# Kernel tuning notes

Measured on AMD Instinct MI355X. Metric: run time of the kernel, lower is better.

The kernel has to match this reference:

```python
import jax, jax.numpy as jnp
import numpy as np

LN_EPS = 1e-5


def _ssm_scan(x_ssm, A, Bm, C, reverse):
    # x_ssm: [B, L, d_inner]; A, Bm, C: [d_inner, d_state]
    Bb, L, di = x_ssm.shape
    ds = Bm.shape[1]

    def step(h, x_t):
        # h: [B, d_inner, d_state], x_t: [B, d_inner]
        h = jnp.clip(h * A[None] + x_t[:, :, None] * Bm[None], -10.0, 10.0)
        y = jnp.einsum('bid,id->bi', h, C)
        return h, y

    h0 = jnp.zeros((Bb, di, ds), x_ssm.dtype)
    _, ys = jax.lax.scan(step, h0, jnp.swapaxes(x_ssm, 0, 1), reverse=reverse)
    return jnp.swapaxes(ys, 0, 1)  # [B, L, d_inner], time-ordered


def setup_inputs() -> dict:
    key = jax.random.key(0)
    ks = jax.random.split(key, 6)
    B, L, D = 4, 2048, 1024
    d_state, expand = 16, 2
    d_inner = D * expand
    x = jax.random.normal(ks[0], (B, L, D), jnp.float32)
    # xavier-ish scaled params
    in_proj_w = jax.random.normal(ks[1], (d_inner * 2, D), jnp.float32) * np.float32(1.0 / np.sqrt(D))
    A_log = jax.random.normal(ks[2], (d_inner, d_state), jnp.float32)
    B_mat = jax.random.normal(ks[3], (d_inner, d_state), jnp.float32) * np.float32(1.0 / np.sqrt(d_state))
    C_mat = jnp.full((d_inner, d_state), 0.01, jnp.float32)
    out_proj_w = jax.random.normal(ks[4], (D, d_inner), jnp.float32) * np.float32(1.0 / np.sqrt(d_inner))
    ln_w = jnp.ones((D,), jnp.float32)
    ln_b = jnp.zeros((D,), jnp.float32)
    return {"x": x, "in_proj_w": in_proj_w, "A_log": A_log, "B_mat": B_mat,
            "C_mat": C_mat, "out_proj_w": out_proj_w, "ln_w": ln_w, "ln_b": ln_b}


def reference(x, in_proj_w, A_log, B_mat, C_mat, out_proj_w, ln_w, ln_b):
    # LayerNorm
    mu = jnp.mean(x, axis=-1, keepdims=True)
    var = jnp.mean((x - mu) ** 2, axis=-1, keepdims=True)
    xn = (x - mu) * jax.lax.rsqrt(var + LN_EPS) * ln_w + ln_b
    # in_proj (no bias), split into ssm stream and gate
    x_proj = jnp.einsum('bld,ed->ble', xn, in_proj_w)  # [B, L, 2*d_inner]
    x_ssm, gate = jnp.split(x_proj, 2, axis=-1)
    # A = -clamp(exp(A_log), -10, -0.01)  (saturates to 0.01, kept faithfully)
    A = -jnp.clip(jnp.exp(A_log), -10.0, -0.01)
    out_f = _ssm_scan(x_ssm, A, B_mat, C_mat, reverse=False)
    out_b = _ssm_scan(x_ssm, A, B_mat, C_mat, reverse=True)
    out = (out_f + out_b) * 0.5 * jax.nn.silu(gate)
    return jnp.einsum('bli,di->bld', out, out_proj_w)
```

## Files before the change

kernel.cpp:

```cpp
#include <hip/hip_runtime.h>

typedef __attribute__((ext_vector_type(8))) _Float16 f16x8;
typedef __attribute__((ext_vector_type(4))) float f32x4;

#define GLOBAL_AS __attribute__((address_space(1)))
#define LDS_AS __attribute__((address_space(3)))

static constexpr int Bb = 4, LL = 2048, DD = 1024, DI = 2048, DS = 16;
static constexpr int MROWS = Bb * LL;
static constexpr int N1 = 2 * DI;
static constexpr int K1 = DD;
static constexpr int N2 = DD;
static constexpr int K2 = DI;

__device__ __forceinline__ unsigned short f2h(float f) {
  _Float16 h = (_Float16)f;
  union { _Float16 h; unsigned short u; } c; c.h = h;
  return c.u;
}
__device__ __forceinline__ float h2f(unsigned short u) {
  union { unsigned short u; _Float16 h; } c; c.u = u;
  return (float)c.h;
}

__global__ __launch_bounds__(256) void ln_half_kernel(
    const float* __restrict__ x, const float* __restrict__ lnw,
    const float* __restrict__ lnb, unsigned short* __restrict__ A1) {
  const int r = blockIdx.x;
  const int tid = threadIdx.x;
  const float4 v = reinterpret_cast<const float4*>(x + (size_t)r * DD)[tid];
  float s = v.x + v.y + v.z + v.w;
#pragma unroll
  for (int off = 32; off >= 1; off >>= 1) s += __shfl_xor(s, off, 64);
  __shared__ float red[8];
  const int wid = tid >> 6;
  if ((tid & 63) == 0) red[wid] = s;
  __syncthreads();
  const float mu = (red[0] + red[1] + red[2] + red[3]) * (1.0f / DD);
  const float dx = v.x - mu, dy = v.y - mu, dz = v.z - mu, dw = v.w - mu;
  float ss = dx * dx + dy * dy + dz * dz + dw * dw;
#pragma unroll
  for (int off = 32; off >= 1; off >>= 1) ss += __shfl_xor(ss, off, 64);
  if ((tid & 63) == 0) red[4 + wid] = ss;
  __syncthreads();
  const float var = (red[4] + red[5] + red[6] + red[7]) * (1.0f / DD);
  const float rs = rsqrtf(var + 1e-5f);
  const float4 w4 = reinterpret_cast<const float4*>(lnw)[tid];
  const float4 b4 = reinterpret_cast<const float4*>(lnb)[tid];
  ushort4 h4;
  h4.x = f2h(dx * rs * w4.x + b4.x);
  h4.y = f2h(dy * rs * w4.y + b4.y);
  h4.z = f2h(dz * rs * w4.z + b4.z);
  h4.w = f2h(dw * rs * w4.w + b4.w);
  *reinterpret_cast<ushort4*>(&A1[(size_t)r * DD + tid * 4]) = h4;
}

__global__ __launch_bounds__(256) void f32_to_f16_kernel(
    const float* __restrict__ W, unsigned short* __restrict__ O) {
  const int gid = blockIdx.x * 256 + threadIdx.x;
  const float4 w = reinterpret_cast<const float4*>(W)[gid];
  ushort4 h4;
  h4.x = f2h(w.x); h4.y = f2h(w.y); h4.z = f2h(w.z); h4.w = f2h(w.w);
  reinterpret_cast<ushort4*>(O)[gid] = h4;
}

__global__ __launch_bounds__(512, 2) void gemm_bt_256(
    const unsigned short* __restrict__ A, const unsigned short* __restrict__ B,
    unsigned short* __restrict__ C, int M, int N, int K) {
  __shared__ unsigned short sm[2][2][256 * 64];
  const int tid = threadIdx.x;
  const int wid = tid >> 6;
  const int lane = tid & 63;
  const int wm = wid >> 2;
  const int wn = wid & 3;
  const int mt = M >> 8;
  const int cpx = gridDim.x >> 3;
  const int bid = blockIdx.x;
  const int sw = (bid & 7) * cpx + (bid >> 3);
  const int bm = sw % mt;
  const int bn = sw / mt;
  const size_t arow0 = (size_t)bm * 256;
  const size_t brow0 = (size_t)bn * 256;

  const unsigned short* gA[4];
  const unsigned short* gB[4];
#pragma unroll
  for (int j = 0; j < 4; ++j) {
    const int idx = j * 512 + tid;
    const int prow = idx >> 3;
    const int scol = ((idx & 7) ^ (prow & 7)) << 3;
    gA[j] = A + (arow0 + prow) * (size_t)K + scol;
    gB[j] = B + (brow0 + prow) * (size_t)K + scol;
  }
  auto stageA = [&](int buf) {
#pragma unroll
    for (int j = 0; j < 4; ++j) {
      __builtin_amdgcn_global_load_lds((const GLOBAL_AS void*)gA[j],
          (LDS_AS void*)&sm[buf][0][(j * 512 + (wid << 6)) * 8], 16, 0, 0);
      gA[j] += 64;
    }
  };
  auto stageB = [&](int buf) {
#pragma unroll
    for (int j = 0; j < 4; ++j) {
      __builtin_amdgcn_global_load_lds((const GLOBAL_AS void*)gB[j],
          (LDS_AS void*)&sm[buf][1][(j * 512 + (wid << 6)) * 8], 16, 0, 0);
      gB[j] += 64;
    }
  };

  const int q = lane >> 4;
  const int l7 = lane & 7;
  const int fr = lane & 15;
  int swz[2];
  swz[0] = (q << 3) ^ (l7 << 3);
  swz[1] = (32 + (q << 3)) ^ (l7 << 3);

  int arows[8], brows[4];
#pragma unroll
  for (int mf = 0; mf < 8; ++mf) arows[mf] = ((wm << 7) + mf * 16 + fr) * 64;
#pragma unroll
  for (int nf = 0; nf < 4; ++nf) brows[nf] = ((wn << 6) + nf * 16 + fr) * 64;

  f32x4 acc[8][4] = {};

  const int NTK = K >> 6;
  stageA(0);
  stageB(0);
  __syncthreads();

  for (int t = 0; t < NTK; ++t) {
    const int cur = t & 1, nxt = cur ^ 1;
    if (t + 1 < NTK) { stageA(nxt); stageB(nxt); }
    f16x8 af[8][2], bf[4][2];
#pragma unroll
    for (int mf = 0; mf < 8; ++mf)
#pragma unroll
      for (int ks = 0; ks < 2; ++ks)
        af[mf][ks] = *reinterpret_cast<const f16x8*>(&sm[cur][0][arows[mf] + swz[ks]]);
#pragma unroll
    for (int nf = 0; nf < 4; ++nf)
#pragma unroll
      for (int ks = 0; ks < 2; ++ks)
        bf[nf][ks] = *reinterpret_cast<const f16x8*>(&sm[cur][1][brows[nf] + swz[ks]]);
#pragma unroll
    for (int ks = 0; ks < 2; ++ks)
#pragma unroll
      for (int mf = 0; mf < 8; ++mf)
#pragma unroll
        for (int nf = 0; nf < 4; ++nf)
          acc[mf][nf] = __builtin_amdgcn_mfma_f32_16x16x32_f16(
              af[mf][ks], bf[nf][ks], acc[mf][nf], 0, 0, 0);
    __syncthreads();
  }

  const int fcol = lane & 15;
  const int frow4 = (lane >> 4) << 2;
#pragma unroll
  for (int mf = 0; mf < 8; ++mf)
#pragma unroll
    for (int nf = 0; nf < 4; ++nf) {
      const size_t row0 = arow0 + (wm << 7) + mf * 16 + frow4;
      const size_t col = brow0 + (wn << 6) + nf * 16 + fcol;
#pragma unroll
      for (int j = 0; j < 4; ++j)
        C[(row0 + j) * (size_t)N + col] = f2h(acc[mf][nf][j]);
    }
}

__global__ __launch_bounds__(512, 2) void gemm_bt_256n128(
    const unsigned short* __restrict__ A, const unsigned short* __restrict__ B,
    float* __restrict__ C, int M, int N, int K) {
  __shared__ unsigned short sm[2][24576];
  const int tid = threadIdx.x;
  const int wid = tid >> 6;
  const int lane = tid & 63;
  const int wm = wid >> 2;
  const int wn = wid & 3;
  const int mt = M >> 8;
  const int cpx = gridDim.x >> 3;
  const int bid = blockIdx.x;
  const int sw = (bid & 7) * cpx + (bid >> 3);
  const int bm = sw % mt;
  const int bn = sw / mt;
  const size_t arow0 = (size_t)bm * 256;
  const size_t brow0 = (size_t)bn * 128;

  const unsigned short* gA[4];
  const unsigned short* gB[2];
#pragma unroll
  for (int j = 0; j < 4; ++j) {
    const int idx = j * 512 + tid;
    const int prow = idx >> 3;
    const int scol = ((idx & 7) ^ (prow & 7)) << 3;
    gA[j] = A + (arow0 + prow) * (size_t)K + scol;
  }
#pragma unroll
  for (int j = 0; j < 2; ++j) {
    const int idx = j * 512 + tid;
    const int prow = idx >> 3;
    const int scol = ((idx & 7) ^ (prow & 7)) << 3;
    gB[j] = B + (brow0 + prow) * (size_t)K + scol;
  }
  auto stageA = [&](int buf) {
#pragma unroll
    for (int j = 0; j < 4; ++j) {
      __builtin_amdgcn_global_load_lds((const GLOBAL_AS void*)gA[j],
          (LDS_AS void*)&sm[buf][(j * 512 + (wid << 6)) * 8], 16, 0, 0);
      gA[j] += 64;
    }
  };
  auto stageB = [&](int buf) {
#pragma unroll
    for (int j = 0; j < 2; ++j) {
      __builtin_amdgcn_global_load_lds((const GLOBAL_AS void*)gB[j],
          (LDS_AS void*)&sm[buf][16384 + (j * 512 + (wid << 6)) * 8], 16, 0, 0);
      gB[j] += 64;
    }
  };

  const int q = lane >> 4;
  const int l7 = lane & 7;
  const int fr = lane & 15;
  int swz[2];
  swz[0] = (q << 3) ^ (l7 << 3);
  swz[1] = (32 + (q << 3)) ^ (l7 << 3);

  int arows[8], brows[2];
#pragma unroll
  for (int mf = 0; mf < 8; ++mf) arows[mf] = ((wm << 7) + mf * 16 + fr) * 64;
#pragma unroll
  for (int nf = 0; nf < 2; ++nf) brows[nf] = 16384 + ((wn << 5) + nf * 16 + fr) * 64;

  f32x4 acc[8][2] = {};

  const int NTK = K >> 6;
  stageA(0);
  stageB(0);
  __syncthreads();

  for (int t = 0; t < NTK; ++t) {
    const int cur = t & 1, nxt = cur ^ 1;
    if (t + 1 < NTK) { stageA(nxt); stageB(nxt); }
    f16x8 af[8][2], bf[2][2];
#pragma unroll
    for (int mf = 0; mf < 8; ++mf)
#pragma unroll
      for (int ks = 0; ks < 2; ++ks)
        af[mf][ks] = *reinterpret_cast<const f16x8*>(&sm[cur][arows[mf] + swz[ks]]);
#pragma unroll
    for (int nf = 0; nf < 2; ++nf)
#pragma unroll
      for (int ks = 0; ks < 2; ++ks)
        bf[nf][ks] = *reinterpret_cast<const f16x8*>(&sm[cur][brows[nf] + swz[ks]]);
#pragma unroll
    for (int ks = 0; ks < 2; ++ks)
#pragma unroll
      for (int mf = 0; mf < 8; ++mf)
#pragma unroll
        for (int nf = 0; nf < 2; ++nf)
          acc[mf][nf] = __builtin_amdgcn_mfma_f32_16x16x32_f16(
              af[mf][ks], bf[nf][ks], acc[mf][nf], 0, 0, 0);
    __syncthreads();
  }

  const int fcol = lane & 15;
  const int frow4 = (lane >> 4) << 2;
#pragma unroll
  for (int mf = 0; mf < 8; ++mf)
#pragma unroll
    for (int nf = 0; nf < 2; ++nf) {
      const size_t row0 = arow0 + (wm << 7) + mf * 16 + frow4;
      const size_t col = brow0 + (wn << 5) + nf * 16 + fcol;
#pragma unroll
      for (int j = 0; j < 4; ++j)
        C[(row0 + j) * (size_t)N + col] = acc[mf][nf][j];
    }
}

__global__ __launch_bounds__(256) void scan_kernel(
    const unsigned short* __restrict__ xp, const float* __restrict__ Bm,
    const float* __restrict__ Cm, unsigned short* __restrict__ oss) {
  constexpr int T = 32, KH = 8;
  const int blk = blockIdx.x;
  const int igrp = blk & 3;
  const int c = (blk >> 2) & 63;
  const int b = blk >> 8;
  const int tid = threadIdx.x;
  const int i0 = igrp * 512 + tid * 2;
  float d0 = 0.f, d1 = 0.f;
#pragma unroll
  for (int ch = 0; ch < 2; ++ch) {
    const float4* bp = reinterpret_cast<const float4*>(Bm + (size_t)(i0 + ch) * DS);
    const float4* cp = reinterpret_cast<const float4*>(Cm + (size_t)(i0 + ch) * DS);
    float d = 0.f;
#pragma unroll
    for (int qv = 0; qv < 4; ++qv) {
      const float4 bv = bp[qv], cv = cp[qv];
      d += bv.x * cv.x + bv.y * cv.y + bv.z * cv.z + bv.w * cv.w;
    }
    if (ch == 0) d0 = d; else d1 = d;
  }
  const float dh0 = 0.5f * d0, dh1 = 0.5f * d1;
  const int t0 = c * T;
  const size_t rowbase = (size_t)b * LL;
  float yf0[T], yf1[T];
  float g0 = 0.f, g1 = 0.f;
  {
    const int hstart = (t0 >= KH) ? t0 - KH : 0;
    for (int t = hstart; t < t0; ++t) {
      const unsigned int u = *reinterpret_cast<const unsigned int*>(
          xp + (rowbase + t) * (size_t)N1 + i0);
      g0 = fmaf(0.01f, g0, h2f((unsigned short)(u & 0xffff)));
      g1 = fmaf(0.01f, g1, h2f((unsigned short)(u >> 16)));
    }
#pragma unroll
    for (int j = 0; j < T; ++j) {
      const unsigned int u = *reinterpret_cast<const unsigned int*>(
          xp + (rowbase + t0 + j) * (size_t)N1 + i0);
      g0 = fmaf(0.01f, g0, h2f((unsigned short)(u & 0xffff)));
      g1 = fmaf(0.01f, g1, h2f((unsigned short)(u >> 16)));
      yf0[j] = g0; yf1[j] = g1;
    }
  }
  g0 = 0.f; g1 = 0.f;
  {
    const int tend = (t0 + T - 1 + KH <= LL - 1) ? (t0 + T - 1 + KH) : (LL - 1);
    for (int t = tend; t >= t0 + T; --t) {
      const unsigned int u = *reinterpret_cast<const unsigned int*>(
          xp + (rowbase + t) * (size_t)N1 + i0);
      g0 = fmaf(0.01f, g0, h2f((unsigned short)(u & 0xffff)));
      g1 = fmaf(0.01f, g1, h2f((unsigned short)(u >> 16)));
    }
#pragma unroll
    for (int j = T - 1; j >= 0; --j) {
      const size_t row = rowbase + t0 + j;
      const unsigned int u = *reinterpret_cast<const unsigned int*>(
          xp + row * (size_t)N1 + i0);
      g0 = fmaf(0.01f, g0, h2f((unsigned short)(u & 0xffff)));
      g1 = fmaf(0.01f, g1, h2f((unsigned short)(u >> 16)));
      const unsigned int ug = *reinterpret_cast<const unsigned int*>(
          xp + row * (size_t)N1 + DI + i0);
      const float gt0 = h2f((unsigned short)(ug & 0xffff));
      const float gt1 = h2f((unsigned short)(ug >> 16));
      const float sg0 = gt0 / (1.f + expf(-gt0));
      const float sg1 = gt1 / (1.f + expf(-gt1));
      const float o0 = (yf0[j] + g0) * dh0 * sg0;
      const float o1 = (yf1[j] + g1) * dh1 * sg1;
      const unsigned int up = (unsigned int)f2h(o0) | ((unsigned int)f2h(o1) << 16);
      *reinterpret_cast<unsigned int*>(oss + row * (size_t)DI + i0) = up;
    }
  }
}

extern "C" void kernel_launch(void* const* d_in, const int* in_sizes, int n_in,
                              void* d_out, int out_size, void* d_ws, size_t ws_size,
                              hipStream_t stream) {
  (void)in_sizes; (void)n_in; (void)out_size; (void)ws_size;
  const float* x          = (const float*)d_in[0];
  const float* in_proj_w  = (const float*)d_in[1];
  const float* B_mat      = (const float*)d_in[3];
  const float* C_mat      = (const float*)d_in[4];
  const float* out_proj_w = (const float*)d_in[5];
  const float* ln_w       = (const float*)d_in[6];
  const float* ln_b       = (const float*)d_in[7];
  float* out = (float*)d_out;

  char* ws = (char*)d_ws;
  unsigned short* A1  = (unsigned short*)ws; ws += (size_t)MROWS * K1 * 2;
  unsigned short* B1  = (unsigned short*)ws; ws += (size_t)N1 * K1 * 2;
  unsigned short* B2  = (unsigned short*)ws; ws += (size_t)N2 * K2 * 2;
  unsigned short* OSS = (unsigned short*)ws; ws += (size_t)MROWS * DI * 2;
  unsigned short* XP  = (unsigned short*)ws; ws += (size_t)MROWS * N1 * 2;

  f32_to_f16_kernel<<<dim3((N1 * K1 / 4) / 256), dim3(256), 0, stream>>>(in_proj_w, B1);
  f32_to_f16_kernel<<<dim3((N2 * K2 / 4) / 256), dim3(256), 0, stream>>>(out_proj_w, B2);
  ln_half_kernel<<<dim3(MROWS), dim3(256), 0, stream>>>(x, ln_w, ln_b, A1);
  gemm_bt_256<<<dim3((MROWS / 256) * (N1 / 256)), dim3(512), 0, stream>>>(A1, B1, XP, MROWS, N1, K1);
  scan_kernel<<<dim3(1024), dim3(256), 0, stream>>>(XP, B_mat, C_mat, OSS);
  gemm_bt_256n128<<<dim3((MROWS / 256) * (N2 / 128)), dim3(512), 0, stream>>>(OSS, B2, out, MROWS, N2, K2);
}
```

Measured before the change: 188.3 us.

## Move linear SSM filter before in_proj and fuse gating into GEMM epilogue

Because the scan is linear and time-invariant, the bidirectional filter is applied to the normalized input (width 1024) before the in-projection instead of to the projected stream (width 2048). The B·C scale is folded into the converted in_proj weights. The new fused GEMM loads both the filtered and unfiltered inputs with a paired weight tile and computes the SiLU gate and product in its epilogue through LDS. This removes the half-precision XP round trip and the separate scan kernel's read of it. In exchange it adds a smaller filter pass and a GEMM that stages three operands per K step.

```diff
diff --git a/kernel.cpp b/kernel.cpp
--- a/kernel.cpp
+++ b/kernel.cpp
@@ -55,6 +55,26 @@
   *reinterpret_cast<ushort4*>(&A1[(size_t)r * DD + tid * 4]) = h4;
 }
 
+__global__ __launch_bounds__(256) void wconv1_kernel(
+    const float* __restrict__ W, const float* __restrict__ Bm,
+    const float* __restrict__ Cm, unsigned short* __restrict__ B1) {
+  const int n = blockIdx.x;
+  const int tid = threadIdx.x;
+  float scale = 1.f;
+  if (n < DI) {
+    float d = 0.f;
+#pragma unroll
+    for (int s = 0; s < DS; ++s)
+      d += Bm[(size_t)n * DS + s] * Cm[(size_t)n * DS + s];
+    scale = 0.5f * d;
+  }
+  const float4 w = reinterpret_cast<const float4*>(W + (size_t)n * DD)[tid];
+  ushort4 h4;
+  h4.x = f2h(w.x * scale); h4.y = f2h(w.y * scale);
+  h4.z = f2h(w.z * scale); h4.w = f2h(w.w * scale);
+  reinterpret_cast<ushort4*>(B1 + (size_t)n * DD)[tid] = h4;
+}
+
 __global__ __launch_bounds__(256) void f32_to_f16_kernel(
     const float* __restrict__ W, unsigned short* __restrict__ O) {
   const int gid = blockIdx.x * 256 + threadIdx.x;
@@ -64,108 +84,179 @@
   reinterpret_cast<ushort4*>(O)[gid] = h4;
 }
 
-__global__ __launch_bounds__(512, 2) void gemm_bt_256(
-    const unsigned short* __restrict__ A, const unsigned short* __restrict__ B,
-    unsigned short* __restrict__ C, int M, int N, int K) {
-  __shared__ unsigned short sm[2][2][256 * 64];
+__global__ __launch_bounds__(256) void filter_kernel(
+    const unsigned short* __restrict__ xn, unsigned short* __restrict__ xs) {
+  constexpr int T = 32, KH = 8;
+  const int blk = blockIdx.x;
+  const int igrp = blk & 1;
+  const int c = (blk >> 1) & 63;
+  const int b = blk >> 7;
+  const int tid = threadIdx.x;
+  const int i0 = igrp * 512 + tid * 2;
+  const int t0 = c * T;
+  const size_t rowbase = (size_t)b * LL;
+  float yf0[T], yf1[T];
+  float g0 = 0.f, g1 = 0.f;
+  {
+    const int hstart = (t0 >= KH) ? t0 - KH : 0;
+    for (int t = hstart; t < t0; ++t) {
+      const unsigned int u = *reinterpret_cast<const unsigned int*>(
+          xn + (rowbase + t) * (size_t)DD + i0);
+      g0 = fmaf(0.01f, g0, h2f((unsigned short)(u & 0xffff)));
+      g1 = fmaf(0.01f, g1, h2f((unsigned short)(u >> 16)));
+    }
+#pragma unroll
+    for (int j = 0; j < T; ++j) {
+      const unsigned int u = *reinterpret_cast<const unsigned int*>(
+          xn + (rowbase + t0 + j) * (size_t)DD + i0);
+      g0 = fmaf(0.01f, g0, h2f((unsigned short)(u & 0xffff)));
+      g1 = fmaf(0.01f, g1, h2f((unsigned short)(u >> 16)));
+      yf0[j] = g0; yf1[j] = g1;
+    }
+  }
+  g0 = 0.f; g1 = 0.f;
+  {
+    const int tend = (t0 + T - 1 + KH <= LL - 1) ? (t0 + T - 1 + KH) : (LL - 1);
+    for (int t = tend; t >= t0 + T; --t) {
+      const unsigned int u = *reinterpret_cast<const unsigned int*>(
+          xn + (rowbase + t) * (size_t)DD + i0);
+      g0 = fmaf(0.01f, g0, h2f((unsigned short)(u & 0xffff)));
+      g1 = fmaf(0.01f, g1, h2f((unsigned short)(u >> 16)));
+    }
+#pragma unroll
+    for (int j = T - 1; j >= 0; --j) {
+      const size_t row = rowbase + t0 + j;
+      const unsigned int u = *reinterpret_cast<const unsigned int*>(
+          xn + row * (size_t)DD + i0);
+      g0 = fmaf(0.01f, g0, h2f((unsigned short)(u & 0xffff)));
+      g1 = fmaf(0.01f, g1, h2f((unsigned short)(u >> 16)));
+      const unsigned int up =
+          (unsigned int)f2h(yf0[j] + g0) | ((unsigned int)f2h(yf1[j] + g1) << 16);
+      *reinterpret_cast<unsigned int*>(xs + row * (size_t)DD + i0) = up;
+    }
+  }
+}
+
+__global__ __launch_bounds__(512, 2) void gemm_fused(
+    const unsigned short* __restrict__ XS, const unsigned short* __restrict__ XN,
+    const unsigned short* __restrict__ W, unsigned short* __restrict__ OSS) {
+  __shared__ unsigned short sm[2][3][8192];
   const int tid = threadIdx.x;
   const int wid = tid >> 6;
   const int lane = tid & 63;
   const int wm = wid >> 2;
   const int wn = wid & 3;
-  const int mt = M >> 8;
+  const int mt = MROWS >> 8;
   const int cpx = gridDim.x >> 3;
   const int bid = blockIdx.x;
   const int sw = (bid & 7) * cpx + (bid >> 3);
   const int bm = sw % mt;
   const int bn = sw / mt;
   const size_t arow0 = (size_t)bm * 256;
-  const size_t brow0 = (size_t)bn * 256;
-
-  const unsigned short* gA[4];
-  const unsigned short* gB[4];
-#pragma unroll
-  for (int j = 0; j < 4; ++j) {
+
+  const unsigned short* gXS[2];
+  const unsigned short* gXN[2];
+  const unsigned short* gW[2];
+#pragma unroll
+  for (int j = 0; j < 2; ++j) {
     const int idx = j * 512 + tid;
-    const int prow = idx >> 3;
-    const int scol = ((idx & 7) ^ (prow & 7)) << 3;
-    gA[j] = A + (arow0 + prow) * (size_t)K + scol;
-    gB[j] = B + (brow0 + prow) * (size_t)K + scol;
-  }
-  auto stageA = [&](int buf) {
-#pragma unroll
-    for (int j = 0; j < 4; ++j) {
-      __builtin_amdgcn_global_load_lds((const GLOBAL_AS void*)gA[j],
-          (LDS_AS void*)&sm[buf][0][(j * 512 + (wid << 6)) * 8], 16, 0, 0);
-      gA[j] += 64;
+    const int prow = idx >> 2;
+    const int scol = ((idx & 3) ^ ((prow >> 1) & 3)) << 3;
+    gXS[j] = XS + (arow0 + prow) * (size_t)K1 + scol;
+    gXN[j] = XN + (arow0 + prow) * (size_t)K1 + scol;
+    const int brow = (prow < 128) ? (bn * 128 + prow)
+                                  : (DI + bn * 128 + (prow - 128));
+    gW[j] = W + (size_t)brow * K1 + scol;
+  }
+  auto stage = [&](int buf) {
+#pragma unroll
+    for (int j = 0; j < 2; ++j) {
+      __builtin_amdgcn_global_load_lds((const GLOBAL_AS void*)gXS[j],
+          (LDS_AS void*)&sm[buf][0][(j * 512 + tid) * 8], 16, 0, 0);
+      gXS[j] += 32;
+    }
+#pragma unroll
+    for (int j = 0; j < 2; ++j) {
+      __builtin_amdgcn_global_load_lds((const GLOBAL_AS void*)gXN[j],
+          (LDS_AS void*)&sm[buf][1][(j * 512 + tid) * 8], 16, 0, 0);
+      gXN[j] += 32;
+    }
+#pragma unroll
+    for (int j = 0; j < 2; ++j) {
+      __builtin_amdgcn_global_load_lds((const GLOBAL_AS void*)gW[j],
+          (LDS_AS void*)&sm[buf][2][(j * 512 + tid) * 8], 16, 0, 0);
+      gW[j] += 32;
     }
   };
-  auto stageB = [&](int buf) {
-#pragma unroll
-    for (int j = 0; j < 4; ++j) {
-      __builtin_amdgcn_global_load_lds((const GLOBAL_AS void*)gB[j],
-          (LDS_AS void*)&sm[buf][1][(j * 512 + (wid << 6)) * 8], 16, 0, 0);
-      gB[j] += 64;
-    }
-  };
 
   const int q = lane >> 4;
-  const int l7 = lane & 7;
   const int fr = lane & 15;
-  int swz[2];
-  swz[0] = (q << 3) ^ (l7 << 3);
-  swz[1] = (32 + (q << 3)) ^ (l7 << 3);
+  const int swzk = ((q ^ ((fr >> 1) & 3)) << 3);
+  const int areg = (wn >= 2) ? 1 : 0;
 
   int arows[8], brows[4];
 #pragma unroll
-  for (int mf = 0; mf < 8; ++mf) arows[mf] = ((wm << 7) + mf * 16 + fr) * 64;
-#pragma unroll
-  for (int nf = 0; nf < 4; ++nf) brows[nf] = ((wn << 6) + nf * 16 + fr) * 64;
+  for (int mf = 0; mf < 8; ++mf) arows[mf] = ((wm << 7) + mf * 16 + fr) * 32;
+#pragma unroll
+  for (int nf = 0; nf < 4; ++nf) brows[nf] = ((wn << 6) + nf * 16 + fr) * 32;
 
   f32x4 acc[8][4] = {};
 
-  const int NTK = K >> 6;
-  stageA(0);
-  stageB(0);
+  const int NTK = K1 >> 5;
+  stage(0);
   __syncthreads();
 
   for (int t = 0; t < NTK; ++t) {
     const int cur = t & 1, nxt = cur ^ 1;
-    if (t + 1 < NTK) { stageA(nxt); stageB(nxt); }
-    f16x8 af[8][2], bf[4][2];
-#pragma unroll
-    for (int mf = 0; mf < 8; ++mf)
-#pragma unroll
-      for (int ks = 0; ks < 2; ++ks)
-        af[mf][ks] = *reinterpret_cast<const f16x8*>(&sm[cur][0][arows[mf] + swz[ks]]);
+    if (t + 1 < NTK) stage(nxt);
+    f16x8 af[8], bf[4];
+#pragma unroll
+    for (int mf = 0; mf < 8; ++mf)
+      af[mf] = *reinterpret_cast<const f16x8*>(&sm[cur][areg][arows[mf] + swzk]);
 #pragma unroll
     for (int nf = 0; nf < 4; ++nf)
-#pragma unroll
-      for (int ks = 0; ks < 2; ++ks)
-        bf[nf][ks] = *reinterpret_cast<const f16x8*>(&sm[cur][1][brows[nf] + swz[ks]]);
-#pragma unroll
-    for (int ks = 0; ks < 2; ++ks)
-#pragma unroll
-      for (int mf = 0; mf < 8; ++mf)
-#pragma unroll
-        for (int nf = 0; nf < 4; ++nf)
-          acc[mf][nf] = __builtin_amdgcn_mfma_f32_16x16x32_f16(
-              af[mf][ks], bf[nf][ks], acc[mf][nf], 0, 0, 0);
+      bf[nf] = *reinterpret_cast<const f16x8*>(&sm[cur][2][brows[nf] + swzk]);
+#pragma unroll
+    for (int mf = 0; mf < 8; ++mf)
+#pragma unroll
+      for (int nf = 0; nf < 4; ++nf)
+        acc[mf][nf] = __builtin_amdgcn_mfma_f32_16x16x32_f16(
+            af[mf], bf[nf], acc[mf][nf], 0, 0, 0);
     __syncthreads();
   }
 
+  unsigned short* gl = &sm[0][0][0];
   const int fcol = lane & 15;
   const int frow4 = (lane >> 4) << 2;
-#pragma unroll
-  for (int mf = 0; mf < 8; ++mf)
-#pragma unroll
-    for (int nf = 0; nf < 4; ++nf) {
-      const size_t row0 = arow0 + (wm << 7) + mf * 16 + frow4;
-      const size_t col = brow0 + (wn << 6) + nf * 16 + fcol;
-#pragma unroll
-      for (int j = 0; j < 4; ++j)
-        C[(row0 + j) * (size_t)N + col] = f2h(acc[mf][nf][j]);
-    }
+  if (wn >= 2) {
+#pragma unroll
+    for (int mf = 0; mf < 8; ++mf)
+#pragma unroll
+      for (int nf = 0; nf < 4; ++nf) {
+        const int gcol = ((wn - 2) << 6) + nf * 16 + fcol;
+        const int r0 = (wm << 7) + mf * 16 + frow4;
+#pragma unroll
+        for (int j = 0; j < 4; ++j) {
+          const float g = acc[mf][nf][j];
+          gl[(r0 + j) * 132 + gcol] = f2h(g / (1.f + expf(-g)));
+        }
+      }
+  }
+  __syncthreads();
+  if (wn < 2) {
+#pragma unroll
+    for (int mf = 0; mf < 8; ++mf)
+#pragma unroll
+      for (int nf = 0; nf < 4; ++nf) {
+        const int scol = (wn << 6) + nf * 16 + fcol;
+        const int r0 = (wm << 7) + mf * 16 + frow4;
+#pragma unroll
+        for (int j = 0; j < 4; ++j) {
+          const float o = acc[mf][nf][j] * h2f(gl[(r0 + j) * 132 + scol]);
+          OSS[(arow0 + r0 + j) * (size_t)DI + bn * 128 + scol] = f2h(o);
+        }
+      }
+  }
 }
 
 __global__ __launch_bounds__(512, 2) void gemm_bt_256n128(
@@ -278,81 +369,6 @@
     }
 }
 
-__global__ __launch_bounds__(256) void scan_kernel(
-    const unsigned short* __restrict__ xp, const float* __restrict__ Bm,
-    const float* __restrict__ Cm, unsigned short* __restrict__ oss) {
-  constexpr int T = 32, KH = 8;
-  const int blk = blockIdx.x;
-  const int igrp = blk & 3;
-  const int c = (blk >> 2) & 63;
-  const int b = blk >> 8;
-  const int tid = threadIdx.x;
-  const int i0 = igrp * 512 + tid * 2;
-  float d0 = 0.f, d1 = 0.f;
-#pragma unroll
-  for (int ch = 0; ch < 2; ++ch) {
-    const float4* bp = reinterpret_cast<const float4*>(Bm + (size_t)(i0 + ch) * DS);
-    const float4* cp = reinterpret_cast<const float4*>(Cm + (size_t)(i0 + ch) * DS);
-    float d = 0.f;
-#pragma unroll
-    for (int qv = 0; qv < 4; ++qv) {
-      const float4 bv = bp[qv], cv = cp[qv];
-      d += bv.x * cv.x + bv.y * cv.y + bv.z * cv.z + bv.w * cv.w;
-    }
-    if (ch == 0) d0 = d; else d1 = d;
-  }
-  const float dh0 = 0.5f * d0, dh1 = 0.5f * d1;
-  const int t0 = c * T;
-  const size_t rowbase = (size_t)b * LL;
-  float yf0[T], yf1[T];
-  float g0 = 0.f, g1 = 0.f;
-  {
-    const int hstart = (t0 >= KH) ? t0 - KH : 0;
-    for (int t = hstart; t < t0; ++t) {
-      const unsigned int u = *reinterpret_cast<const unsigned int*>(
-          xp + (rowbase + t) * (size_t)N1 + i0);
-      g0 = fmaf(0.01f, g0, h2f((unsigned short)(u & 0xffff)));
-      g1 = fmaf(0.01f, g1, h2f((unsigned short)(u >> 16)));
-    }
-#pragma unroll
-    for (int j = 0; j < T; ++j) {
-      const unsigned int u = *reinterpret_cast<const unsigned int*>(
-          xp + (rowbase + t0 + j) * (size_t)N1 + i0);
-      g0 = fmaf(0.01f, g0, h2f((unsigned short)(u & 0xffff)));
-      g1 = fmaf(0.01f, g1, h2f((unsigned short)(u >> 16)));
-      yf0[j] = g0; yf1[j] = g1;
-    }
-  }
-  g0 = 0.f; g1 = 0.f;
-  {
-    const int tend = (t0 + T - 1 + KH <= LL - 1) ? (t0 + T - 1 + KH) : (LL - 1);
-    for (int t = tend; t >= t0 + T; --t) {
-      const unsigned int u = *reinterpret_cast<const unsigned int*>(
-          xp + (rowbase + t) * (size_t)N1 + i0);
-      g0 = fmaf(0.01f, g0, h2f((unsigned short)(u & 0xffff)));
-      g1 = fmaf(0.01f, g1, h2f((unsigned short)(u >> 16)));
-    }
-#pragma unroll
-    for (int j = T - 1; j >= 0; --j) {
-      const size_t row = rowbase + t0 + j;
-      const unsigned int u = *reinterpret_cast<const unsigned int*>(
-          xp + row * (size_t)N1 + i0);
-      g0 = fmaf(0.01f, g0, h2f((unsigned short)(u & 0xffff)));
-      g1 = fmaf(0.01f, g1, h2f((unsigned short)(u >> 16)));
-      const unsigned int ug = *reinterpret_cast<const unsigned int*>(
-          xp + row * (size_t)N1 + DI + i0);
-      const float gt0 = h2f((unsigned short)(ug & 0xffff));
-      const float gt1 = h2f((unsigned short)(ug >> 16));
-      const float sg0 = gt0 / (1.f + expf(-gt0));
-      const float sg1 = gt1 / (1.f + expf(-gt1));
-      const float o0 = (yf0[j] + g0) * dh0 * sg0;
-      const float o1 = (yf1[j] + g1) * dh1 * sg1;
-      const unsigned int up = (unsigned int)f2h(o0) | ((unsigned int)f2h(o1) << 16);
-      *reinterpret_cast<unsigned int*>(oss + row * (size_t)DI + i0) = up;
-    }
-  }
-}
-
 extern "C" void kernel_launch(void* const* d_in, const int* in_sizes, int n_in,
                               void* d_out, int out_size, void* d_ws, size_t ws_size,
                               hipStream_t stream) {
@@ -371,12 +387,12 @@
   unsigned short* B1  = (unsigned short*)ws; ws += (size_t)N1 * K1 * 2;
   unsigned short* B2  = (unsigned short*)ws; ws += (size_t)N2 * K2 * 2;
   unsigned short* OSS = (unsigned short*)ws; ws += (size_t)MROWS * DI * 2;
-  unsigned short* XP  = (unsigned short*)ws; ws += (size_t)MROWS * N1 * 2;
-
-  f32_to_f16_kernel<<<dim3((N1 * K1 / 4) / 256), dim3(256), 0, stream>>>(in_proj_w, B1);
+  unsigned short* XS  = (unsigned short*)ws; ws += (size_t)MROWS * K1 * 2;
+
+  wconv1_kernel<<<dim3(N1), dim3(256), 0, stream>>>(in_proj_w, B_mat, C_mat, B1);
   f32_to_f16_kernel<<<dim3((N2 * K2 / 4) / 256), dim3(256), 0, stream>>>(out_proj_w, B2);
   ln_half_kernel<<<dim3(MROWS), dim3(256), 0, stream>>>(x, ln_w, ln_b, A1);
-  gemm_bt_256<<<dim3((MROWS / 256) * (N1 / 256)), dim3(512), 0, stream>>>(A1, B1, XP, MROWS, N1, K1);
-  scan_kernel<<<dim3(1024), dim3(256), 0, stream>>>(XP, B_mat, C_mat, OSS);
+  filter_kernel<<<dim3(512), dim3(256), 0, stream>>>(A1, XS);
+  gemm_fused<<<dim3((MROWS / 256) * (DI / 128)), dim3(512), 0, stream>>>(XS, A1, B1, OSS);
   gemm_bt_256n128<<<dim3((MROWS / 256) * (N2 / 128)), dim3(512), 0, stream>>>(OSS, B2, out, MROWS, N2, K2);
 }
```

Result: slower. 193.6 us (+2.8%).
